# Optimization experiments

Measured on AMD Instinct MI355X. Metric: run time of the kernel, lower is better.

## Reference

```python
import jax, jax.numpy as jnp
import numpy as np

K = 3
KK = K * K


def conv3x3(x, w, b):
    # x: [B,C,H,W], w: [O,C,3,3]
    y = jax.lax.conv_general_dilated(x, w, (1, 1), ((1, 1), (1, 1)),
                                     dimension_numbers=('NCHW', 'OIHW', 'NCHW'))
    return y + b[None, :, None, None]


def deform_conv(x, offset, w, b):
    # torchvision.ops.deform_conv2d, 3x3, pad=1, stride=1, no mask.
    B, C, H, W = x.shape
    off = offset.reshape(B, KK, 2, H, W)  # per kernel tap: (dy, dx)
    ky = jnp.repeat(jnp.arange(K, dtype=x.dtype) - 1, K)  # [9]
    kx = jnp.tile(jnp.arange(K, dtype=x.dtype) - 1, K)
    py = jnp.arange(H, dtype=x.dtype)[None, None, :, None] + ky[None, :, None, None] + off[:, :, 0]
    px = jnp.arange(W, dtype=x.dtype)[None, None, None, :] + kx[None, :, None, None] + off[:, :, 1]
    y0 = jnp.floor(py)
    x0 = jnp.floor(px)
    wy = (py - y0)[:, None]  # [B,1,9,H,W]
    wx = (px - x0)[:, None]
    y0i = y0.astype(jnp.int32)
    x0i = x0.astype(jnp.int32)
    xf = x.reshape(B, C, H * W)

    def corner(yi, xi):
        valid = ((yi >= 0) & (yi < H) & (xi >= 0) & (xi < W))
        idx = jnp.clip(yi, 0, H - 1) * W + jnp.clip(xi, 0, W - 1)  # [B,9,H,W]
        g = jax.vmap(lambda xb, ib: xb[:, ib.reshape(-1)])(xf, idx)  # [B,C,9*H*W]
        return g.reshape(B, C, KK, H, W) * valid[:, None].astype(x.dtype)

    val = (corner(y0i, x0i) * (1 - wy) * (1 - wx)
           + corner(y0i, x0i + 1) * (1 - wy) * wx
           + corner(y0i + 1, x0i) * wy * (1 - wx)
           + corner(y0i + 1, x0i + 1) * wy * wx)  # [B,C,9,H,W]
    out = jnp.einsum('bckhw,ock->bohw', val, w.reshape(w.shape[0], C, KK))
    return out + b[None, :, None, None]


def se_gate(x, w1, b1, w2, b2):
    # global avg pool -> 1x1 conv -> relu -> 1x1 conv -> sigmoid -> scale
    m = x.mean((2, 3))  # [B,C]
    h = jax.nn.relu(jnp.einsum('bc,rc->br', m, w1) + b1)
    g = jax.nn.sigmoid(jnp.einsum('br,cr->bc', h, w2) + b2)
    return x * g[:, :, None, None]


def resize_bilinear(x, oh, ow):
    # F.interpolate(mode='bilinear', align_corners=False)
    B, C, H, W = x.shape

    def coords(n_in, n_out):
        src = (jnp.arange(n_out, dtype=x.dtype) + 0.5) * (n_in / n_out) - 0.5
        src = jnp.clip(src, 0.0, n_in - 1)
        i0 = jnp.floor(src).astype(jnp.int32)
        i1 = jnp.minimum(i0 + 1, n_in - 1)
        return i0, i1, (src - i0).astype(x.dtype)

    y0, y1, wy = coords(H, oh)
    x = x[:, :, y0, :] * (1 - wy)[None, None, :, None] + x[:, :, y1, :] * wy[None, None, :, None]
    c0, c1, wc = coords(W, ow)
    x = x[:, :, :, c0] * (1 - wc)[None, None, None, :] + x[:, :, :, c1] * wc[None, None, None, :]
    return x


def setup_inputs() -> dict:
    key = jax.random.key(0)
    ks = jax.random.split(key, 12)
    B, C, H, W = 4, 64, 128, 128
    L, O, R = 4, 64, 4  # levels, out_channels, reduction=64//16
    d = {
        'x': jax.random.normal(ks[0], (B, C, H, W), jnp.float32),
        'off_w': jax.random.normal(ks[1], (L, 2 * KK, C, 3, 3), jnp.float32) * 0.01,
        'off_b': jax.random.normal(ks[2], (L, 2 * KK), jnp.float32) * 0.01,
        'dc_w': jax.random.normal(ks[3], (L, O, C, 3, 3), jnp.float32) * 0.05,
        'dc_b': jax.random.normal(ks[4], (L, O), jnp.float32) * 0.05,
        'se_w1': jax.random.normal(ks[5], (L, R, O), jnp.float32) * 0.1,
        'se_b1': jax.random.normal(ks[6], (L, R), jnp.float32) * 0.1,
        'se_w2': jax.random.normal(ks[7], (L, O, R), jnp.float32) * 0.1,
        'se_b2': jax.random.normal(ks[8], (L, O), jnp.float32) * 0.1,
        'fuse_w': jax.random.normal(ks[9], (O, L * O), jnp.float32) * 0.05,
        'fuse_b': jax.random.normal(ks[10], (O,), jnp.float32) * 0.05,
    }
    return d


def reference(x, off_w, off_b, dc_w, dc_b, se_w1, se_b1, se_w2, se_b2, fuse_w, fuse_b):
    B, _, H, W = x.shape
    L = off_w.shape[0]
    cur = x
    feats = []
    for i in range(L):
        if i > 0:
            cur = resize_bilinear(cur, cur.shape[2] // 2, cur.shape[3] // 2)
        off = conv3x3(cur, off_w[i], off_b[i])
        cur = deform_conv(cur, off, dc_w[i], dc_b[i])
        cur = se_gate(cur, se_w1[i], se_b1[i], se_w2[i], se_b2[i])
        feats.append(resize_bilinear(cur, H, W))
    for i in range(L - 2, -1, -1):
        feats[i] = feats[i] + feats[i + 1]
    fused = jnp.concatenate(feats, axis=1)  # [B, L*O, H, W]
    return jnp.einsum('bchw,oc->bohw', fused, fuse_w) + fuse_b[None, :, None, None]
```

## Files before the change

kernel.cpp:

```cpp
#include <hip/hip_runtime.h>
#include <hip/hip_bf16.h>
#include <math.h>


constexpr int Bn = 4;

typedef __attribute__((ext_vector_type(8))) short short8;
typedef __attribute__((ext_vector_type(4))) float f32x4;
typedef __attribute__((ext_vector_type(4))) unsigned uint4v;
typedef __attribute__((ext_vector_type(4))) unsigned short ushort4v;

static __device__ __forceinline__ short f2b(float f){
  union { float f; unsigned u; } v; v.f = f;
  unsigned r = v.u + 0x7fffu + ((v.u >> 16) & 1u);
  return (short)(r >> 16);
}
static __device__ __forceinline__ unsigned f2b2(float x, float y){
  union { __hip_bfloat162 h; unsigned u; } cv;
  cv.h = __float22bfloat162_rn(make_float2(x, y));
  return cv.u;
}
static __device__ __forceinline__ float blo(unsigned u){ return __uint_as_float(u << 16); }
static __device__ __forceinline__ float bhi(unsigned u){ return __uint_as_float(u & 0xffff0000u); }
static __device__ __forceinline__ void pinv(uint4v& x){ asm volatile("" : "+v"(x)); }

constexpr size_t OFF_CUR   = 0;
constexpr size_t OFF_DC    = OFF_CUR  + 4194304;
constexpr size_t OFF_T0    = OFF_DC   + 4194304;
constexpr size_t OFF_T1    = OFF_T0   + 4194304;
constexpr size_t OFF_T2    = OFF_T1   + 1048576;
constexpr size_t OFF_T3    = OFF_T2   + 262144;
constexpr size_t OFF_WSUMT = OFF_T3   + 65536;
constexpr size_t OFF_DCWT  = OFF_WSUMT + 8192;
constexpr size_t OFF_OWT   = OFF_DCWT  + 73728;
constexpr size_t OFF_SUMS  = OFF_OWT   + 36864;

__global__ void prep_k(const float* __restrict__ dc_w, const float* __restrict__ off_w,
                       const float* __restrict__ fuse_w, float* __restrict__ ws){
  int i = blockIdx.x * 256 + threadIdx.x;
  short* dcwT  = (short*)(ws + OFF_DCWT);
  short* owT   = (short*)(ws + OFF_OWT);
  short* wsumT = (short*)(ws + OFF_WSUMT);
  if (i < 147456){
    int oc = i / 576, r = i % 576, k = r >> 6, c = r & 63;
    dcwT[i] = f2b(dc_w[(oc*64 + c)*9 + k]);
  } else if (i < 147456 + 73728){
    int t = i - 147456;
    int lm = t / 576, l = lm >> 5, m = lm & 31, r = t % 576, k = r >> 6, c = r & 63;
    owT[t] = (m < 18) ? f2b(off_w[((l*18 + m)*64 + c)*9 + k]) : (short)0;
  } else if (i < 147456 + 73728 + 16384){
    int t = i - (147456 + 73728);
    int l = t / 4096, r = t % 4096, o = r / 64, c = r % 64;
    float s = 0.f;
    for (int jl = 0; jl <= l; jl++) s += fuse_w[o*256 + jl*64 + c];
    wsumT[t] = f2b(s);
  } else if (i < 147456 + 73728 + 16384 + 65536){
    ws[OFF_SUMS + (i - (147456 + 73728 + 16384))] = 0.f;
  }
}

__global__ __launch_bounds__(256) void cvt_k(const float* __restrict__ x, unsigned* __restrict__ cur){
  __shared__ float t[64][65];
  int tile = blockIdx.x;
  int b = tile >> 8, p0 = (tile & 255) << 6;
  int tx = threadIdx.x & 63, ty = threadIdx.x >> 6;
  #pragma unroll
  for (int c = ty; c < 64; c += 4)
    t[c][tx] = x[(((size_t)(b << 6) + c) << 14) + p0 + tx];
  __syncthreads();
  int u = threadIdx.x & 31, pr = threadIdx.x >> 5;
  #pragma unroll
  for (int i = 0; i < 8; i++){
    int pp = pr + i*8;
    unsigned v = f2b2(t[2*u][pp], t[2*u + 1][pp]);
    cur[((size_t)(b << 14) + p0 + pp)*32 + u] = v;
  }
}

template<int H, int LVL>
__global__ __launch_bounds__(256, 3) void deform8_k(
    const unsigned* __restrict__ cur, const float* __restrict__ ws_all,
    const float* __restrict__ off_bias, const float* __restrict__ dc_bias,
    float* __restrict__ dc, float* __restrict__ sums){
  constexpr int W = H, P = H * W;
  constexpr int PITCHB = 584 * 2;
  constexpr int TPR8 = W/8, TPB8 = P/64;
  __shared__ __align__(16) short valA[16][584];
  __shared__ __align__(16) char  patchS[64*144];
  __shared__ __align__(16) float4 tapW[144];
  __shared__ __align__(8)  unsigned short tapIs[144][4];
  float* offsP = (float*)((char*)&valA[0][0] + 8192);
  const short* owt = (const short*)(ws_all + OFF_OWT) + LVL * 32 * 576;
  const short* dcw = (const short*)(ws_all + OFF_DCWT) + (size_t)LVL * 64 * 576;
  const int tid = threadIdx.x;
  const int wave = tid >> 6, lane = tid & 63;
  const int c0 = lane & 15, quad = lane >> 4, q4 = quad * 4;
  const int b = blockIdx.x / TPB8;
  const int rr = blockIdx.x % TPB8;
  const int hrow8 = (rr / TPR8) * 8, wcol8 = (rr % TPR8) * 8;
  const unsigned* curu = cur + (size_t)b * P * 32;

  uint4v wB[9];
  {
    const short* wrow = owt + ((wave & 1)*16 + c0)*576 + quad*8;
    #pragma unroll
    for (int kb = 0; kb < 9; kb++)
      wB[kb] = *(const uint4v*)&wrow[((wave >> 1)*9 + kb)*32];
    #pragma unroll
    for (int kb = 0; kb < 9; kb++) pinv(wB[kb]);
  }
  const int n = wave*16 + c0;
  uint4v wD[18];
  #pragma unroll
  for (int kb = 0; kb < 18; kb++)
    wD[kb] = *(const uint4v*)&dcw[n*576 + kb*32 + quad*8];
  #pragma unroll
  for (int kb = 0; kb < 18; kb++) pinv(wD[kb]);
  const float bt2 = dc_bias[LVL*64 + n];
  const int tk = tid % 9, tp = tid / 9;
  float oby = 0.f, obx = 0.f;
  if (tid < 144){
    oby = off_bias[LVL*18 + 2*tk];
    obx = off_bias[LVL*18 + 2*tk + 1];
  }
  const int pl = lane >> 3, cq = lane & 7;

  #pragma unroll 1
  for (int t = 0; t < 4; t++){
    const int srow = hrow8 + (t >> 1)*4, scol = wcol8 + (t & 1)*4;
    if (t) __syncthreads();

    #pragma unroll
    for (int i = 0; i < 2; i++){
      int pp = wave*16 + i*8 + pl;
      int R = pp >> 3, C = pp & 7;
      int yy = srow - 2 + R, xx = scol - 2 + C;
      bool v = ((unsigned)yy < (unsigned)H) & ((unsigned)xx < (unsigned)W);
      int idx = v ? (yy*W + xx) : 0;
      uint4 d = *(const uint4*)((const char*)curu + (size_t)idx*128 + cq*16);
      if (!v){ d.x = 0; d.y = 0; d.z = 0; d.w = 0; }
      *(uint4*)(patchS + pp*144 + cq*16) = d;
    }
    __syncthreads();

    {
      const int colw = wave & 1, kh = wave >> 1;
      const char* pb = patchS + (((c0 >> 2) + 1)*8 + (c0 & 3) + 1)*144 + quad*16;
      f32x4 oacc = {0,0,0,0};
      if (kh == 0){
        #pragma unroll
        for (int kb = 0; kb < 9; kb++){
          const int tap = kb >> 1;
          short8 a = *(const short8*)(pb + ((tap/3)*8 + (tap%3))*144 + (kb&1)*64);
          oacc = __builtin_amdgcn_mfma_f32_16x16x32_bf16(a, __builtin_bit_cast(short8, wB[kb]), oacc, 0, 0, 0);
        }
      } else {
        #pragma unroll
        for (int kb = 0; kb < 9; kb++){
          const int kk = 9 + kb, tap = kk >> 1;
          short8 a = *(const short8*)(pb + ((tap/3)*8 + (tap%3))*144 + (kk&1)*64);
          oacc = __builtin_amdgcn_mfma_f32_16x16x32_bf16(a, __builtin_bit_cast(short8, wB[kb]), oacc, 0, 0, 0);
        }
      }
      int comp = colw*16 + c0;
      if (comp < 18){
        #pragma unroll
        for (int r = 0; r < 4; r++) offsP[kh*288 + (q4 + r)*18 + comp] = oacc[r];
      }
    }
    __syncthreads();

    if (tid < 144){
      int p = tp, k = tk;
      int h = srow + (p >> 2), w = scol + (p & 3);
      float oy = offsP[p*18 + 2*k]     + offsP[288 + p*18 + 2*k]     + oby;
      float ox = offsP[p*18 + 2*k + 1] + offsP[288 + p*18 + 2*k + 1] + obx;
      float py = (float)(h + k/3 - 1) + oy;
      float px = (float)(w + k%3 - 1) + ox;
      float y0f = floorf(py), x0f = floorf(px);
      float fy = py - y0f, fx = px - x0f;
      int y0 = (int)y0f, x0 = (int)x0f, y1 = y0 + 1, x1 = x0 + 1;
      bool vy0 = (y0 >= 0) & (y0 < H), vy1 = (y1 >= 0) & (y1 < H);
      bool vx0 = (x0 >= 0) & (x0 < W), vx1 = (x1 >= 0) & (x1 < W);
      int y0c = min(max(y0, 0), H-1), y1c = min(max(y1, 0), H-1);
      int x0c = min(max(x0, 0), W-1), x1c = min(max(x1, 0), W-1);
      float gy = 1.f - fy, gx = 1.f - fx;
      tapW[tid] = make_float4((vy0 & vx0) ? gy*gx : 0.f,
                              (vy0 & vx1) ? gy*fx : 0.f,
                              (vy1 & vx0) ? fy*gx : 0.f,
                              (vy1 & vx1) ? fy*fx : 0.f);
      int ry = y0 - srow + 2, rx = x0 - scol + 2;
      if (((unsigned)ry < 7u) & ((unsigned)rx < 7u)){
        tapIs[tid][0] = (unsigned short)(0x8000u | (ry*8 + rx));
      } else {
        tapIs[tid][0] = (unsigned short)(y0c*W + x0c);
        tapIs[tid][1] = (unsigned short)(y0c*W + x1c);
        tapIs[tid][2] = (unsigned short)(y1c*W + x0c);
        tapIs[tid][3] = (unsigned short)(y1c*W + x1c);
      }
    }
    __syncthreads();

    {
      const char* curc8 = (const char*)curu + c0*8;
      int T = wave*36 + quad;
      int p = wave*4, k = quad;
      #pragma unroll
      for (int i = 0; i < 9; i++){
        float4 wv = tapW[T];
        unsigned short t0 = tapIs[T][0];
        uint2 u0, u1, u2, u3;
        if (t0 & 0x8000u){
          const char* pb2 = patchS + (int)(t0 & 0x7fffu)*144 + c0*8;
          u0 = *(const uint2*)(pb2);
          u1 = *(const uint2*)(pb2 + 144);
          u2 = *(const uint2*)(pb2 + 144*8);
          u3 = *(const uint2*)(pb2 + 144*9);
        } else {
          uint2 tw = *(const uint2*)tapIs[T];
          u0 = *(const uint2*)(curc8 + ((size_t)(tw.x & 0xffffu) << 7));
          u1 = *(const uint2*)(curc8 + ((size_t)(tw.x >> 16)     << 7));
          u2 = *(const uint2*)(curc8 + ((size_t)(tw.y & 0xffffu) << 7));
          u3 = *(const uint2*)(curc8 + ((size_t)(tw.y >> 16)     << 7));
        }
        float a0 = wv.x*blo(u0.x) + wv.y*blo(u1.x) + wv.z*blo(u2.x) + wv.w*blo(u3.x);
        float a1 = wv.x*bhi(u0.x) + wv.y*bhi(u1.x) + wv.z*bhi(u2.x) + wv.w*bhi(u3.x);
        float a2 = wv.x*blo(u0.y) + wv.y*blo(u1.y) + wv.z*blo(u2.y) + wv.w*blo(u3.y);
        float a3 = wv.x*bhi(u0.y) + wv.y*bhi(u1.y) + wv.z*bhi(u2.y) + wv.w*bhi(u3.y);
        uint2 pk; pk.x = f2b2(a0, a1); pk.y = f2b2(a2, a3);
        *(uint2*)((char*)&valA[0][0] + p*PITCHB + k*128 + c0*8) = pk;
        T += 4; k += 4; if (k >= 9){ k -= 9; ++p; }
      }
    }
    __syncthreads();

    f32x4 d0 = {bt2, bt2, bt2, bt2}, d1 = {0,0,0,0};
    #pragma unroll
    for (int kb = 0; kb < 9; kb++){
      short8 a = *(const short8*)&valA[c0][kb*32 + quad*8];
      d0 = __builtin_amdgcn_mfma_f32_16x16x32_bf16(a, __builtin_bit_cast(short8, wD[kb]), d0, 0, 0, 0);
    }
    #pragma unroll
    for (int kb = 9; kb < 18; kb++){
      short8 a = *(const short8*)&valA[c0][kb*32 + quad*8];
      d1 = __builtin_amdgcn_mfma_f32_16x16x32_bf16(a, __builtin_bit_cast(short8, wD[kb]), d1, 0, 0, 0);
    }
    f32x4 acc;
    #pragma unroll
    for (int r = 0; r < 4; r++) acc[r] = d0[r] + d1[r];
    float* dcb = dc + ((size_t)b*P + (size_t)(srow + quad)*W + scol)*64;
    #pragma unroll
    for (int r = 0; r < 4; r++) dcb[r*64 + n] = acc[r];
    float s = acc[0] + acc[1] + acc[2] + acc[3];
    s += __shfl_xor(s, 16);
    s += __shfl_xor(s, 32);
    if (quad == 0) atomicAdd(&sums[(LVL*16 + (blockIdx.x & 15))*256 + (b << 6) + n], s);
  }
}

template<int H, int LVL>
__global__ __launch_bounds__(256, 7) void deform_k(
    const unsigned* __restrict__ cur, const float* __restrict__ ws_all,
    const float* __restrict__ off_bias, const float* __restrict__ dc_bias,
    float* __restrict__ dc, float* __restrict__ sums){
  constexpr int W = H, P = H * W;
  constexpr int PITCHB = 584 * 2;
  constexpr int TPR = W/4, TPB = P/16;
  __shared__ __align__(16) short valA[16][584];
  __shared__ __align__(16) float4 tapW[144];
  __shared__ __align__(8)  unsigned short tapIs[144][4];
  short* patch = &valA[0][0];
  float* offsP = (float*)((char*)&valA[0][0] + 8192);
  const short* owt = (const short*)(ws_all + OFF_OWT) + LVL * 32 * 576;
  const short* dcw = (const short*)(ws_all + OFF_DCWT) + (size_t)LVL * 64 * 576;
  const int tid = threadIdx.x;
  const int wave = tid >> 6, lane = tid & 63;
  const int c0 = lane & 15, quad = lane >> 4, q4 = quad * 4;
  const int b = blockIdx.x / TPB;
  const int rr = blockIdx.x % TPB;
  const int hrow = (rr / TPR) * 4, wcol = (rr % TPR) * 4;
  const unsigned* curu = cur + (size_t)b * P * 32;

  {
    #pragma unroll
    for (int i = 0; i < 3; i++){
      if (i < 2 || quad == 0){
        int p36 = wave*9 + i*4 + quad;
        int r6 = p36 / 6, c6 = p36 - r6*6;
        int yy = hrow - 1 + r6, xx = wcol - 1 + c6;
        bool v = ((unsigned)yy < (unsigned)H) & ((unsigned)xx < (unsigned)W);
        int idx = v ? (yy*W + xx) : 0;
        uint2 d = *(const uint2*)(curu + (size_t)idx*32 + c0*2);
        if (!v){ d.x = 0u; d.y = 0u; }
        *(uint2*)(patch + p36*72 + c0*4) = d;
      }
    }
  }
  __syncthreads();

  {
    const int colw = wave & 1, kh = wave >> 1;
    const char* pb = (const char*)patch + ((c0 >> 2) * 6 + (c0 & 3)) * 144 + quad * 16;
    const short* wrow = owt + (colw*16 + c0)*576 + quad*8;
    f32x4 oacc = {0,0,0,0};
    if (kh == 0){
      #pragma unroll
      for (int kb = 0; kb < 9; kb++){
        const int tap = kb >> 1;
        short8 a  = *(const short8*)(pb + ((tap/3)*864 + (tap%3)*144 + (kb&1)*64));
        short8 bf = *(const short8*)&wrow[kb*32];
        oacc = __builtin_amdgcn_mfma_f32_16x16x32_bf16(a, bf, oacc, 0, 0, 0);
      }
    } else {
      #pragma unroll
      for (int kb = 0; kb < 9; kb++){
        const int kk = 9 + kb, tap = kk >> 1;
        short8 a  = *(const short8*)(pb + ((tap/3)*864 + (tap%3)*144 + (kk&1)*64));
        short8 bf = *(const short8*)&wrow[kk*32];
        oacc = __builtin_amdgcn_mfma_f32_16x16x32_bf16(a, bf, oacc, 0, 0, 0);
      }
    }
    int comp = colw*16 + c0;
    if (comp < 18){
      #pragma unroll
      for (int r = 0; r < 4; r++) offsP[kh*288 + (q4 + r)*18 + comp] = oacc[r];
    }
  }
  __syncthreads();

  if (tid < 144){
    int p = tid / 9, k = tid % 9;
    int h = hrow + (p >> 2), w = wcol + (p & 3);
    float oy = offsP[p*18 + 2*k]     + offsP[288 + p*18 + 2*k]     + off_bias[LVL*18 + 2*k];
    float ox = offsP[p*18 + 2*k + 1] + offsP[288 + p*18 + 2*k + 1] + off_bias[LVL*18 + 2*k + 1];
    float py = (float)(h + k/3 - 1) + oy;
    float px = (float)(w + k%3 - 1) + ox;
    float y0f = floorf(py), x0f = floorf(px);
    float fy = py - y0f, fx = px - x0f;
    int y0 = (int)y0f, x0 = (int)x0f, y1 = y0 + 1, x1 = x0 + 1;
    bool vy0 = (y0 >= 0) & (y0 < H), vy1 = (y1 >= 0) & (y1 < H);
    bool vx0 = (x0 >= 0) & (x0 < W), vx1 = (x1 >= 0) & (x1 < W);
    int y0c = min(max(y0, 0), H-1), y1c = min(max(y1, 0), H-1);
    int x0c = min(max(x0, 0), W-1), x1c = min(max(x1, 0), W-1);
    float gy = 1.f - fy, gx = 1.f - fx;
    tapW[tid] = make_float4((vy0 & vx0) ? gy*gx : 0.f,
                            (vy0 & vx1) ? gy*fx : 0.f,
                            (vy1 & vx0) ? fy*gx : 0.f,
                            (vy1 & vx1) ? fy*fx : 0.f);
    ushort4v ti = { (unsigned short)(y0c*W + x0c), (unsigned short)(y0c*W + x1c),
                    (unsigned short)(y1c*W + x0c), (unsigned short)(y1c*W + x1c) };
    *(ushort4v*)tapIs[tid] = ti;
  }
  __syncthreads();

  {
    const char* curc8 = (const char*)curu + c0*8;
    int T = wave*36 + quad;
    int p = T/9, k = T - p*9;
    #pragma unroll
    for (int i = 0; i < 9; i++){
      float4 wv = tapW[T];
      uint2 tw = *(const uint2*)tapIs[T];
      uint2 u0 = *(const uint2*)(curc8 + ((size_t)(tw.x & 0xffffu) << 7));
      uint2 u1 = *(const uint2*)(curc8 + ((size_t)(tw.x >> 16) << 7));
      uint2 u2 = *(const uint2*)(curc8 + ((size_t)(tw.y & 0xffffu) << 7));
      uint2 u3 = *(const uint2*)(curc8 + ((size_t)(tw.y >> 16) << 7));
      float a0 = wv.x*blo(u0.x) + wv.y*blo(u1.x) + wv.z*blo(u2.x) + wv.w*blo(u3.x);
      float a1 = wv.x*bhi(u0.x) + wv.y*bhi(u1.x) + wv.z*bhi(u2.x) + wv.w*bhi(u3.x);
      float a2 = wv.x*blo(u0.y) + wv.y*blo(u1.y) + wv.z*blo(u2.y) + wv.w*blo(u3.y);
      float a3 = wv.x*bhi(u0.y) + wv.y*bhi(u1.y) + wv.z*bhi(u2.y) + wv.w*bhi(u3.y);
      uint2 pk; pk.x = f2b2(a0, a1); pk.y = f2b2(a2, a3);
      *(uint2*)((char*)&valA[0][0] + p*PITCHB + k*128 + c0*8) = pk;
      T += 4; k += 4; if (k >= 9){ k -= 9; ++p; }
    }
  }
  __syncthreads();

  const int n = wave*16 + c0;
  float bt2 = dc_bias[LVL*64 + n];
  f32x4 d0 = {bt2, bt2, bt2, bt2}, d1 = {0,0,0,0};
  #pragma unroll
  for (int kb = 0; kb < 9; kb++){
    short8 a  = *(const short8*)&valA[c0][kb*32 + quad*8];
    short8 bf = *(const short8*)&dcw[n*576 + kb*32 + quad*8];
    d0 = __builtin_amdgcn_mfma_f32_16x16x32_bf16(a, bf, d0, 0, 0, 0);
  }
  #pragma unroll
  for (int kb = 9; kb < 18; kb++){
    short8 a  = *(const short8*)&valA[c0][kb*32 + quad*8];
    short8 bf = *(const short8*)&dcw[n*576 + kb*32 + quad*8];
    d1 = __builtin_amdgcn_mfma_f32_16x16x32_bf16(a, bf, d1, 0, 0, 0);
  }
  f32x4 acc;
  #pragma unroll
  for (int r = 0; r < 4; r++) acc[r] = d0[r] + d1[r];
  float* dcb = dc + ((size_t)b*P + (size_t)(hrow + quad)*W + wcol)*64;
  #pragma unroll
  for (int r = 0; r < 4; r++) dcb[r*64 + n] = acc[r];
  float s = acc[0] + acc[1] + acc[2] + acc[3];
  s += __shfl_xor(s, 16);
  s += __shfl_xor(s, 32);
  if (quad == 0) atomicAdd(&sums[(LVL*16 + (blockIdx.x & 15))*256 + (b << 6) + n], s);
}

template<int W, int LVL>
__global__ __launch_bounds__(256) void fuse_gd_k(
    const float* __restrict__ dcv, const float* __restrict__ sums,
    const float* __restrict__ se_w1, const float* __restrict__ se_b1,
    const float* __restrict__ se_w2, const float* __restrict__ se_b2,
    const float* __restrict__ ws_all, float* __restrict__ tmp, unsigned* __restrict__ curn){
  constexpr int P = W * W;
  constexpr bool POOL = (LVL < 3);
  constexpr float invP = 1.f / (float)P;
  __shared__ __align__(16) float fS[64][68];
  __shared__ __align__(16) float gsh[64];
  const short* wsl = (const short*)(ws_all + OFF_WSUMT) + LVL * 4096;
  const int tid = threadIdx.x, wave = tid >> 6, lane = tid & 63;
  const int c0 = lane & 15, quad = lane >> 4, q4 = quad * 4;
  int b, rp = 0, cs = 0;
  if (POOL){
    constexpr int tilesPerB = P / 64, tilesPerRow = W / 32;
    b = blockIdx.x / tilesPerB;
    int r = blockIdx.x % tilesPerB;
    rp = r / tilesPerRow; cs = r % tilesPerRow;
  } else {
    b = (blockIdx.x * 64) / P;
  }

  {
    int sg = tid >> 6, c = tid & 63;
    float part = 0.f;
    #pragma unroll
    for (int s = 0; s < 4; s++) part += sums[(LVL*16 + sg*4 + s)*256 + (b << 6) + c];
    fS[sg][c] = part;
    __syncthreads();
    if (tid < 64){
      int r = tid & 3, j = tid >> 2;
      float hp = 0.f;
      #pragma unroll
      for (int q = 0; q < 4; q++){
        int cq = j*4 + q;
        float m = (fS[0][cq] + fS[1][cq] + fS[2][cq] + fS[3][cq]) * invP;
        hp += m * se_w1[(LVL*4 + r)*64 + cq];
      }
      hp += __shfl_xor(hp, 4);  hp += __shfl_xor(hp, 8);
      hp += __shfl_xor(hp, 16); hp += __shfl_xor(hp, 32);
      float hr = fmaxf(hp + se_b1[LVL*4 + r], 0.f);
      float a = se_b2[LVL*64 + tid];
      #pragma unroll
      for (int r2 = 0; r2 < 4; r2++)
        a += __shfl(hr, r2) * se_w2[(LVL*64 + tid)*4 + r2];
      gsh[tid] = 1.f / (1.f + expf(-a));
    }
    __syncthreads();
  }

  float4 g4 = *(const float4*)&gsh[c0*4];
  #pragma unroll
  for (int i = 0; i < 4; i++){
    int lp = wave*16 + (lane >> 4) + i*4;
    size_t gpix = POOL ? ((size_t)b*P + (size_t)(2*rp + (lp >> 5))*W + cs*32 + (lp & 31))
                       : ((size_t)blockIdx.x*64 + lp);
    float4 d = *(const float4*)&dcv[gpix*64 + c0*4];
    float4 v = make_float4(d.x*g4.x, d.y*g4.y, d.z*g4.z, d.w*g4.w);
    *(float4*)&fS[lp][c0*4] = v;
  }
  __syncthreads();
  f32x4 acc[4] = {{0,0,0,0},{0,0,0,0},{0,0,0,0},{0,0,0,0}};
  #pragma unroll
  for (int kb = 0; kb < 2; kb++){
    float4 lo = *(const float4*)&fS[wave*16 + c0][kb*32 + quad*8];
    float4 hi = *(const float4*)&fS[wave*16 + c0][kb*32 + quad*8 + 4];
    uint4v ua = {f2b2(lo.x, lo.y), f2b2(lo.z, lo.w), f2b2(hi.x, hi.y), f2b2(hi.z, hi.w)};
    short8 a = __builtin_bit_cast(short8, ua);
    #pragma unroll
    for (int t = 0; t < 4; t++){
      short8 bf = *(const short8*)&wsl[(t*16 + c0)*64 + kb*32 + quad*8];
      acc[t] = __builtin_amdgcn_mfma_f32_16x16x32_bf16(a, bf, acc[t], 0, 0, 0);
    }
  }
  #pragma unroll
  for (int t = 0; t < 4; t++){
    int n = t*16 + c0;
    size_t plane = ((size_t)(b << 6) + n) * P;
    size_t pix = POOL ? ((size_t)(2*rp + (wave >> 1))*W + cs*32 + (wave & 1)*16 + q4)
                      : ((size_t)(blockIdx.x*64) - (size_t)b*P + wave*16 + q4);
    *(f32x4*)&tmp[plane + pix] = acc[t];
  }
  if constexpr (POOL){
    int j = tid >> 4, uu = tid & 15;
    float4 p0 = *(const float4*)&fS[2*j][uu*4];
    float4 p1 = *(const float4*)&fS[2*j + 1][uu*4];
    float4 p2 = *(const float4*)&fS[32 + 2*j][uu*4];
    float4 p3 = *(const float4*)&fS[33 + 2*j][uu*4];
    float4 av = make_float4(0.25f*(p0.x + p1.x + p2.x + p3.x),
                            0.25f*(p0.y + p1.y + p2.y + p3.y),
                            0.25f*(p0.z + p1.z + p2.z + p3.z),
                            0.25f*(p0.w + p1.w + p2.w + p3.w));
    uint2 pv = make_uint2(f2b2(av.x, av.y), f2b2(av.z, av.w));
    *(uint2*)&curn[((size_t)b*(P/4) + (size_t)rp*(W/2) + cs*16 + j)*32 + uu*2] = pv;
  }
}

__global__ void final_k(const float* __restrict__ ws_all, const float* __restrict__ fuse_bias,
                        float* __restrict__ out){
  int i = blockIdx.x * 256 + threadIdx.x;
  int w = i & 127, h = (i >> 7) & 127, o = (i >> 14) & 63, b = i >> 20;
  float acc = fuse_bias[o] + ws_all[OFF_T0 + (((size_t)(b << 6) + o) << 14) + (h << 7) + w];
  const float* tarr[3] = {ws_all + OFF_T1, ws_all + OFF_T2, ws_all + OFF_T3};
  #pragma unroll
  for (int li = 0; li < 3; li++){
    int l = li + 1, Hl = 128 >> l;
    float scale = 1.0f / (float)(1 << l);
    float sy = fminf(fmaxf((h + 0.5f)*scale - 0.5f, 0.f), (float)(Hl - 1));
    float sx = fminf(fmaxf((w + 0.5f)*scale - 0.5f, 0.f), (float)(Hl - 1));
    int y0 = (int)sy, x0 = (int)sx;
    float fy = sy - y0, fx = sx - x0;
    int y1 = min(y0 + 1, Hl - 1), x1 = min(x0 + 1, Hl - 1);
    const float* tb = tarr[li] + (size_t)((b << 6) + o) * Hl * Hl;
    float v00 = tb[y0*Hl + x0], v01 = tb[y0*Hl + x1];
    float v10 = tb[y1*Hl + x0], v11 = tb[y1*Hl + x1];
    acc += (1.f-fy)*((1.f-fx)*v00 + fx*v01) + fy*((1.f-fx)*v10 + fx*v11);
  }
  out[i] = acc;
}

extern "C" void kernel_launch(void* const* d_in, const int* in_sizes, int n_in,
                              void* d_out, int out_size, void* d_ws, size_t ws_size,
                              hipStream_t stream){
  (void)in_sizes; (void)n_in; (void)out_size; (void)ws_size;
  const float* x      = (const float*)d_in[0];
  const float* off_w  = (const float*)d_in[1];
  const float* off_b  = (const float*)d_in[2];
  const float* dc_w   = (const float*)d_in[3];
  const float* dc_b   = (const float*)d_in[4];
  const float* se_w1  = (const float*)d_in[5];
  const float* se_b1  = (const float*)d_in[6];
  const float* se_w2  = (const float*)d_in[7];
  const float* se_b2  = (const float*)d_in[8];
  const float* fuse_w = (const float*)d_in[9];
  const float* fuse_b = (const float*)d_in[10];
  float* out = (float*)d_out;
  float* ws = (float*)d_ws;
  unsigned* cur = (unsigned*)(ws + OFF_CUR);
  float* dc   = ws + OFF_DC;
  float* tmp[4] = {ws + OFF_T0, ws + OFF_T1, ws + OFF_T2, ws + OFF_T3};
  float* sums = ws + OFF_SUMS;

  prep_k<<<(303104 + 255)/256, 256, 0, stream>>>(dc_w, off_w, fuse_w, ws);
  cvt_k<<<1024, 256, 0, stream>>>(x, cur);

  deform8_k<128,0><<<1024, 256, 0, stream>>>(cur, ws, off_b, dc_b, dc, sums);
  fuse_gd_k<128,0><<<1024, 256, 0, stream>>>(dc, sums, se_w1, se_b1, se_w2, se_b2, ws, tmp[0], cur);
  deform_k<64,1><<<1024, 256, 0, stream>>>(cur, ws, off_b, dc_b, dc, sums);
  fuse_gd_k<64,1><<<256, 256, 0, stream>>>(dc, sums, se_w1, se_b1, se_w2, se_b2, ws, tmp[1], cur);
  deform_k<32,2><<<256, 256, 0, stream>>>(cur, ws, off_b, dc_b, dc, sums);
  fuse_gd_k<32,2><<<64, 256, 0, stream>>>(dc, sums, se_w1, se_b1, se_w2, se_b2, ws, tmp[2], cur);
  deform_k<16,3><<<64, 256, 0, stream>>>(cur, ws, off_b, dc_b, dc, sums);
  fuse_gd_k<16,3><<<16, 256, 0, stream>>>(dc, sums, se_w1, se_b1, se_w2, se_b2, ws, tmp[3], nullptr);

  final_k<<<16384, 256, 0, stream>>>(ws, fuse_b, out);
}
```

Measured before the change: 228.5 us.

## Merge prep and convert kernels; load deform weights per use instead of pinning

Combines the weight-preparation kernel and the input NCHW-to-bf16 conversion kernel into one launch, saving a kernel launch and its gap. In the level-0 deform kernel, the offset-conv and deform-conv B fragments are no longer preloaded into pinned registers. They are reloaded from global memory next to each MFMA. This lowers register pressure, which may help occupancy or cut spills, at the cost of repeated global/L2 loads inside the tile loop.

```diff
diff --git a/kernel.cpp b/kernel.cpp
--- a/kernel.cpp
+++ b/kernel.cpp
@@ -22,7 +22,6 @@
 }
 static __device__ __forceinline__ float blo(unsigned u){ return __uint_as_float(u << 16); }
 static __device__ __forceinline__ float bhi(unsigned u){ return __uint_as_float(u & 0xffff0000u); }
-static __device__ __forceinline__ void pinv(uint4v& x){ asm volatile("" : "+v"(x)); }
 
 constexpr size_t OFF_CUR   = 0;
 constexpr size_t OFF_DC    = OFF_CUR  + 4194304;
@@ -35,45 +34,48 @@
 constexpr size_t OFF_OWT   = OFF_DCWT  + 73728;
 constexpr size_t OFF_SUMS  = OFF_OWT   + 36864;
 
-__global__ void prep_k(const float* __restrict__ dc_w, const float* __restrict__ off_w,
-                       const float* __restrict__ fuse_w, float* __restrict__ ws){
-  int i = blockIdx.x * 256 + threadIdx.x;
-  short* dcwT  = (short*)(ws + OFF_DCWT);
-  short* owT   = (short*)(ws + OFF_OWT);
-  short* wsumT = (short*)(ws + OFF_WSUMT);
-  if (i < 147456){
-    int oc = i / 576, r = i % 576, k = r >> 6, c = r & 63;
-    dcwT[i] = f2b(dc_w[(oc*64 + c)*9 + k]);
-  } else if (i < 147456 + 73728){
-    int t = i - 147456;
-    int lm = t / 576, l = lm >> 5, m = lm & 31, r = t % 576, k = r >> 6, c = r & 63;
-    owT[t] = (m < 18) ? f2b(off_w[((l*18 + m)*64 + c)*9 + k]) : (short)0;
-  } else if (i < 147456 + 73728 + 16384){
-    int t = i - (147456 + 73728);
-    int l = t / 4096, r = t % 4096, o = r / 64, c = r % 64;
-    float s = 0.f;
-    for (int jl = 0; jl <= l; jl++) s += fuse_w[o*256 + jl*64 + c];
-    wsumT[t] = f2b(s);
-  } else if (i < 147456 + 73728 + 16384 + 65536){
-    ws[OFF_SUMS + (i - (147456 + 73728 + 16384))] = 0.f;
-  }
-}
-
-__global__ __launch_bounds__(256) void cvt_k(const float* __restrict__ x, unsigned* __restrict__ cur){
+__global__ __launch_bounds__(256) void prepcvt_k(
+    const float* __restrict__ dc_w, const float* __restrict__ off_w,
+    const float* __restrict__ fuse_w, float* __restrict__ ws,
+    const float* __restrict__ x, unsigned* __restrict__ cur){
   __shared__ float t[64][65];
-  int tile = blockIdx.x;
-  int b = tile >> 8, p0 = (tile & 255) << 6;
-  int tx = threadIdx.x & 63, ty = threadIdx.x >> 6;
-  #pragma unroll
-  for (int c = ty; c < 64; c += 4)
-    t[c][tx] = x[(((size_t)(b << 6) + c) << 14) + p0 + tx];
-  __syncthreads();
-  int u = threadIdx.x & 31, pr = threadIdx.x >> 5;
-  #pragma unroll
-  for (int i = 0; i < 8; i++){
-    int pp = pr + i*8;
-    unsigned v = f2b2(t[2*u][pp], t[2*u + 1][pp]);
-    cur[((size_t)(b << 14) + p0 + pp)*32 + u] = v;
+  {
+    int i = blockIdx.x * 256 + threadIdx.x;
+    short* dcwT  = (short*)(ws + OFF_DCWT);
+    short* owT   = (short*)(ws + OFF_OWT);
+    short* wsumT = (short*)(ws + OFF_WSUMT);
+    if (i < 147456){
+      int oc = i / 576, r = i % 576, k = r >> 6, c = r & 63;
+      dcwT[i] = f2b(dc_w[(oc*64 + c)*9 + k]);
+    } else if (i < 147456 + 73728){
+      int tt = i - 147456;
+      int lm = tt / 576, l = lm >> 5, m = lm & 31, r = tt % 576, k = r >> 6, c = r & 63;
+      owT[tt] = (m < 18) ? f2b(off_w[((l*18 + m)*64 + c)*9 + k]) : (short)0;
+    } else if (i < 147456 + 73728 + 16384){
+      int tt = i - (147456 + 73728);
+      int l = tt / 4096, r = tt % 4096, o = r / 64, c = r % 64;
+      float s = 0.f;
+      for (int jl = 0; jl <= l; jl++) s += fuse_w[o*256 + jl*64 + c];
+      wsumT[tt] = f2b(s);
+    } else if (i < 147456 + 73728 + 16384 + 65536){
+      ws[OFF_SUMS + (i - (147456 + 73728 + 16384))] = 0.f;
+    }
+  }
+  if (blockIdx.x < 1024){
+    int tile = blockIdx.x;
+    int b = tile >> 8, p0 = (tile & 255) << 6;
+    int tx = threadIdx.x & 63, ty = threadIdx.x >> 6;
+    #pragma unroll
+    for (int c = ty; c < 64; c += 4)
+      t[c][tx] = x[(((size_t)(b << 6) + c) << 14) + p0 + tx];
+    __syncthreads();
+    int u = threadIdx.x & 31, pr = threadIdx.x >> 5;
+    #pragma unroll
+    for (int i = 0; i < 8; i++){
+      int pp = pr + i*8;
+      unsigned v = f2b2(t[2*u][pp], t[2*u + 1][pp]);
+      cur[((size_t)(b << 14) + p0 + pp)*32 + u] = v;
+    }
   }
 }
 
@@ -99,23 +101,7 @@
   const int rr = blockIdx.x % TPB8;
   const int hrow8 = (rr / TPR8) * 8, wcol8 = (rr % TPR8) * 8;
   const unsigned* curu = cur + (size_t)b * P * 32;
-
-  uint4v wB[9];
-  {
-    const short* wrow = owt + ((wave & 1)*16 + c0)*576 + quad*8;
-    #pragma unroll
-    for (int kb = 0; kb < 9; kb++)
-      wB[kb] = *(const uint4v*)&wrow[((wave >> 1)*9 + kb)*32];
-    #pragma unroll
-    for (int kb = 0; kb < 9; kb++) pinv(wB[kb]);
-  }
   const int n = wave*16 + c0;
-  uint4v wD[18];
-  #pragma unroll
-  for (int kb = 0; kb < 18; kb++)
-    wD[kb] = *(const uint4v*)&dcw[n*576 + kb*32 + quad*8];
-  #pragma unroll
-  for (int kb = 0; kb < 18; kb++) pinv(wD[kb]);
   const float bt2 = dc_bias[LVL*64 + n];
   const int tk = tid % 9, tp = tid / 9;
   float oby = 0.f, obx = 0.f;
@@ -146,20 +132,23 @@
     {
       const int colw = wave & 1, kh = wave >> 1;
       const char* pb = patchS + (((c0 >> 2) + 1)*8 + (c0 & 3) + 1)*144 + quad*16;
+      const short* wrow = owt + (colw*16 + c0)*576 + quad*8;
       f32x4 oacc = {0,0,0,0};
       if (kh == 0){
         #pragma unroll
         for (int kb = 0; kb < 9; kb++){
           const int tap = kb >> 1;
-          short8 a = *(const short8*)(pb + ((tap/3)*8 + (tap%3))*144 + (kb&1)*64);
-          oacc = __builtin_amdgcn_mfma_f32_16x16x32_bf16(a, __builtin_bit_cast(short8, wB[kb]), oacc, 0, 0, 0);
+          short8 a  = *(const short8*)(pb + ((tap/3)*8 + (tap%3))*144 + (kb&1)*64);
+          short8 bf = *(const short8*)&wrow[kb*32];
+          oacc = __builtin_amdgcn_mfma_f32_16x16x32_bf16(a, bf, oacc, 0, 0, 0);
         }
       } else {
         #pragma unroll
         for (int kb = 0; kb < 9; kb++){
           const int kk = 9 + kb, tap = kk >> 1;
-          short8 a = *(const short8*)(pb + ((tap/3)*8 + (tap%3))*144 + (kk&1)*64);
-          oacc = __builtin_amdgcn_mfma_f32_16x16x32_bf16(a, __builtin_bit_cast(short8, wB[kb]), oacc, 0, 0, 0);
+          short8 a  = *(const short8*)(pb + ((tap/3)*8 + (tap%3))*144 + (kk&1)*64);
+          short8 bf = *(const short8*)&wrow[kk*32];
+          oacc = __builtin_amdgcn_mfma_f32_16x16x32_bf16(a, bf, oacc, 0, 0, 0);
         }
       }
       int comp = colw*16 + c0;
@@ -237,13 +226,15 @@
     f32x4 d0 = {bt2, bt2, bt2, bt2}, d1 = {0,0,0,0};
     #pragma unroll
     for (int kb = 0; kb < 9; kb++){
-      short8 a = *(const short8*)&valA[c0][kb*32 + quad*8];
-      d0 = __builtin_amdgcn_mfma_f32_16x16x32_bf16(a, __builtin_bit_cast(short8, wD[kb]), d0, 0, 0, 0);
+      short8 a  = *(const short8*)&valA[c0][kb*32 + quad*8];
+      short8 bf = *(const short8*)&dcw[n*576 + kb*32 + quad*8];
+      d0 = __builtin_amdgcn_mfma_f32_16x16x32_bf16(a, bf, d0, 0, 0, 0);
     }
     #pragma unroll
     for (int kb = 9; kb < 18; kb++){
-      short8 a = *(const short8*)&valA[c0][kb*32 + quad*8];
-      d1 = __builtin_amdgcn_mfma_f32_16x16x32_bf16(a, __builtin_bit_cast(short8, wD[kb]), d1, 0, 0, 0);
+      short8 a  = *(const short8*)&valA[c0][kb*32 + quad*8];
+      short8 bf = *(const short8*)&dcw[n*576 + kb*32 + quad*8];
+      d1 = __builtin_amdgcn_mfma_f32_16x16x32_bf16(a, bf, d1, 0, 0, 0);
     }
     f32x4 acc;
     #pragma unroll
@@ -547,8 +538,7 @@
   float* tmp[4] = {ws + OFF_T0, ws + OFF_T1, ws + OFF_T2, ws + OFF_T3};
   float* sums = ws + OFF_SUMS;
 
-  prep_k<<<(303104 + 255)/256, 256, 0, stream>>>(dc_w, off_w, fuse_w, ws);
-  cvt_k<<<1024, 256, 0, stream>>>(x, cur);
+  prepcvt_k<<<(303104 + 255)/256, 256, 0, stream>>>(dc_w, off_w, fuse_w, ws, x, cur);
 
   deform8_k<128,0><<<1024, 256, 0, stream>>>(cur, ws, off_b, dc_b, dc, sums);
   fuse_gd_k<128,0><<<1024, 256, 0, stream>>>(dc, sums, se_w1, se_b1, se_w2, se_b2, ws, tmp[0], cur);
```

Measured after the change: 219.5 us. 1.04x faster.
